# Kernel tuning notes

Hardware: AMD Instinct MI355X
Metric: run time of the kernel (lower is better)

Reference implementation:

```python
import jax, jax.numpy as jnp
import numpy as np

B, S, T, V, E, H, D, A = 16, 128, 128, 32000, 512, 512, 512, 512
ENC = 2 * H  # bidirectional encoder output dim
NEG = -1e9


def _w(key, shape, scale=0.05):
    return scale * jax.random.normal(key, shape, dtype=jnp.float32)


def setup_inputs() -> dict:
    key = jax.random.key(0)
    ks = jax.random.split(key, 26)
    src = jax.random.randint(ks[0], (B, S), 1, V)
    tgt = jax.random.randint(ks[1], (B, T), 1, V)
    src_lens = jnp.full((B,), S, dtype=jnp.int32)  # full-length sequences (pack == identity)
    return dict(
        src=src, src_lens=src_lens, tgt=tgt,
        enc_embed=_w(ks[2], (V, E)).at[0].set(0.0),   # padding_idx=0
        Wih_f=_w(ks[3], (4 * H, E)), Whh_f=_w(ks[4], (4 * H, H)),
        bih_f=_w(ks[5], (4 * H,)), bhh_f=_w(ks[6], (4 * H,)),
        Wih_b=_w(ks[7], (4 * H, E)), Whh_b=_w(ks[8], (4 * H, H)),
        bih_b=_w(ks[9], (4 * H,)), bhh_b=_w(ks[10], (4 * H,)),
        Wbh=_w(ks[11], (D, 2 * H)), bbh=_w(ks[12], (D,)),
        Wbc=_w(ks[13], (D, 2 * H)), bbc=_w(ks[14], (D,)),
        Wh_att=_w(ks[15], (A, ENC)), Ws_att=_w(ks[16], (A, D)), v_att=_w(ks[17], (A,)),
        dec_embed=_w(ks[18], (V, E)).at[0].set(0.0),  # padding_idx=0
        Wih_d=_w(ks[19], (4 * D, E + ENC)), Whh_d=_w(ks[20], (4 * D, D)),
        bih_d=_w(ks[21], (4 * D,)), bhh_d=_w(ks[22], (4 * D,)),
        Wfc=_w(ks[23], (V, D + ENC)), bfc=_w(ks[24], (V,)),
    )


def _lstm_cell(x, h, c, Wih, Whh, bih, bhh):
    # PyTorch gate order: i, f, g, o
    g = x @ Wih.T + h @ Whh.T + (bih + bhh)
    i, f, gg, o = jnp.split(g, 4, axis=-1)
    c = jax.nn.sigmoid(f) * c + jax.nn.sigmoid(i) * jnp.tanh(gg)
    h = jax.nn.sigmoid(o) * jnp.tanh(c)
    return h, c


def _run_lstm(xs, Wih, Whh, bih, bhh, hdim):
    # xs: [S, B, E] -> (hs [S, B, hdim], h_last, c_last)
    b = xs.shape[1]
    h0 = jnp.zeros((b, hdim), xs.dtype)

    def step(carry, x):
        h, c = carry
        h, c = _lstm_cell(x, h, c, Wih, Whh, bih, bhh)
        return (h, c), h

    (hT, cT), hs = jax.lax.scan(step, (h0, h0), xs)
    return hs, hT, cT


def reference(src, src_lens, tgt, enc_embed, Wih_f, Whh_f, bih_f, bhh_f,
              Wih_b, Whh_b, bih_b, bhh_b, Wbh, bbh, Wbc, bbc,
              Wh_att, Ws_att, v_att, dec_embed, Wih_d, Whh_d, bih_d, bhh_d,
              Wfc, bfc):
    # ---- BiLSTM encoder (src_lens == S, so packing is the identity) ----
    emb = enc_embed[src]                      # [B, S, E]
    xs = jnp.swapaxes(emb, 0, 1)              # [S, B, E]
    hs_f, hf, _ = _run_lstm(xs, Wih_f, Whh_f, bih_f, bhh_f, H)
    hs_b, hb, _ = _run_lstm(xs[::-1], Wih_b, Whh_b, bih_b, bhh_b, H)
    hs_b = hs_b[::-1]
    enc_out = jnp.swapaxes(jnp.concatenate([hs_f, hs_b], axis=-1), 0, 1)  # [B, S, 2H]

    # ---- bridge (num_layers = 1) ----
    h_cat = jnp.concatenate([hf, hb], axis=-1)  # [B, 2H]
    h0 = jnp.tanh(h_cat @ Wbh.T + bbh)          # [B, D]
    c_cat = jnp.concatenate([hf, hb], axis=-1)
    c0 = jnp.tanh(c_cat @ Wbc.T + bbc)

    mask = jnp.arange(S)[None, :] < src_lens[:, None]  # [B, S]
    enc_proj = jnp.einsum('bse,ae->bsa', enc_out, Wh_att)  # W_h(enc_out), hoisted

    # ---- decoder loop, teacher_forcing = 1.0 ----
    def dec_step(carry, inp_t):
        h, c = carry
        # Bahdanau attention on top-layer hidden state
        score = jnp.einsum('bsa,a->bs', jnp.tanh(enc_proj + (h @ Ws_att.T)[:, None, :]), v_att)
        score = jnp.where(mask, score, NEG)
        attn = jax.nn.softmax(score, axis=-1)
        ctx = jnp.einsum('bs,bse->be', attn, enc_out)       # [B, 2H]
        x = jnp.concatenate([dec_embed[inp_t], ctx], axis=-1)  # [B, E+2H]
        h, c = _lstm_cell(x, h, c, Wih_d, Whh_d, bih_d, bhh_d)
        logits = jnp.concatenate([h, ctx], axis=-1) @ Wfc.T + bfc  # [B, V]
        return (h, c), logits

    inps = tgt[:, :-1].T  # [T-1, B]
    _, logits = jax.lax.scan(dec_step, (h0, c0), inps)
    return jnp.swapaxes(logits, 0, 1)  # [B, T-1, V]
```

## Files before the change

### kernel.cpp

```cpp
#include <hip/hip_runtime.h>

typedef __bf16 bf16x8 __attribute__((ext_vector_type(8)));
typedef float f32x4 __attribute__((ext_vector_type(4)));
typedef unsigned short us;
typedef unsigned long long ull;

#define DEV static __device__ __forceinline__

DEV float bf2f(us u){ union { unsigned u; float f; } x; x.u = ((unsigned)u) << 16; return x.f; }
DEV us f2bf(float f){
  union { float f; unsigned u; } x; x.f = f;
  unsigned r = x.u + 0x7fffu + ((x.u >> 16) & 1u);
  return (us)(r >> 16);
}
DEV unsigned pack2(us lo, us hi){ return (unsigned)lo | ((unsigned)hi << 16); }
DEV float sigm(float x){ return 1.0f / (1.0f + expf(-x)); }
DEV float tanh_fast(float x){ float e = __expf(2.0f * x); return 1.0f - 2.0f / (e + 1.0f); }
DEV void unpk2(unsigned u, float& a, float& b){ a = bf2f((us)u); b = bf2f((us)(u >> 16)); }

DEV unsigned ld4v(const unsigned* p){ return __hip_atomic_load(p, __ATOMIC_RELAXED, __HIP_MEMORY_SCOPE_AGENT); }
DEV ull ld8v(const void* p){ return __hip_atomic_load((const ull*)p, __ATOMIC_RELAXED, __HIP_MEMORY_SCOPE_AGENT); }
DEV void st4v(unsigned* p, unsigned v){ __hip_atomic_store(p, v, __ATOMIC_RELAXED, __HIP_MEMORY_SCOPE_AGENT); }

DEV void gridbar3(unsigned* arr, unsigned ep){
  __syncthreads();
  if (threadIdx.x == 0)
    __hip_atomic_store(arr + (size_t)blockIdx.x * 16, ep, __ATOMIC_RELEASE, __HIP_MEMORY_SCOPE_AGENT);
  if (threadIdx.x < 128){
    while (__hip_atomic_load(arr + (size_t)threadIdx.x * 16, __ATOMIC_RELAXED, __HIP_MEMORY_SCOPE_AGENT) < ep)
      __builtin_amdgcn_s_sleep(4);
  }
  __syncthreads();
}

DEV void groupbar(unsigned* gbase, int slot, unsigned ep){
  __syncthreads();
  if (threadIdx.x == 0)
    __hip_atomic_store(gbase + slot * 16, ep, __ATOMIC_RELEASE, __HIP_MEMORY_SCOPE_AGENT);
  if (threadIdx.x < 8){
    while (__hip_atomic_load(gbase + threadIdx.x * 16, __ATOMIC_RELAXED, __HIP_MEMORY_SCOPE_AGENT) < ep)
      __builtin_amdgcn_s_sleep(2);
  }
  __syncthreads();
}

__global__ void k_f2bf(const float4* __restrict__ in, uint2* __restrict__ out, long n4){
  long stride = (long)gridDim.x * blockDim.x;
  for (long i = (long)blockIdx.x * blockDim.x + threadIdx.x; i < n4; i += stride){
    float4 v = in[i];
    uint2 o; o.x = pack2(f2bf(v.x), f2bf(v.y)); o.y = pack2(f2bf(v.z), f2bf(v.w));
    out[i] = o;
  }
}

__global__ void k_bias3(const float* a0, const float* b0, float* o0,
                        const float* a1, const float* b1, float* o1,
                        const float* a2, const float* b2, float* o2){
  int i = blockIdx.x * 256 + threadIdx.x;
  o0[i] = a0[i] + b0[i];
  o1[i] = a1[i] + b1[i];
  o2[i] = a2[i] + b2[i];
}

__global__ void k_embed(const int* __restrict__ tok, const float* __restrict__ table,
                        us* __restrict__ out){
  int r = blockIdx.x;
  int b = r & 15, pos = r >> 4;
  int idx = tok[b * 128 + pos];
  float4 v = ((const float4*)(table + (size_t)idx * 512))[threadIdx.x];
  uint2 o; o.x = pack2(f2bf(v.x), f2bf(v.y)); o.y = pack2(f2bf(v.z), f2bf(v.w));
  ((uint2*)(out + (size_t)r * 512))[threadIdx.x] = o;
}

template<int MODE>
__global__ __launch_bounds__(256)
void gemm_bt(const us* __restrict__ A, int lda,
             const us* __restrict__ B, int ldb,
             const float* __restrict__ bias,
             void* __restrict__ Cv, int ldc, int K, int mvalid)
{
  __shared__ __align__(16) us As[128 * 64];
  __shared__ __align__(16) us Bs[128 * 64];
  const int tid  = threadIdx.x;
  const int lane = tid & 63, wid = tid >> 6;
  const int wm = (wid >> 1) * 64, wn = (wid & 1) * 64;
  const us* Ab = A + (size_t)blockIdx.y * 128 * lda;
  const us* Bb = B + (size_t)blockIdx.x * 128 * ldb;

  f32x4 acc[4][4] = {};
  bf16x8 ga[4], gb[4];

  #pragma unroll
  for (int r = 0; r < 4; r++){
    int c = tid + r * 256;
    ga[r] = *(const bf16x8*)(Ab + (size_t)(c >> 3) * lda + (c & 7) * 8);
    gb[r] = *(const bf16x8*)(Bb + (size_t)(c >> 3) * ldb + (c & 7) * 8);
  }
  const int nt = K >> 6;
  for (int t = 0; t < nt; t++){
    #pragma unroll
    for (int r = 0; r < 4; r++){
      int c = tid + r * 256;
      int slot = ((c >> 3) * 8 + ((c & 7) ^ ((c >> 3) & 7))) * 8;
      *(bf16x8*)(As + slot) = ga[r];
      *(bf16x8*)(Bs + slot) = gb[r];
    }
    __syncthreads();
    if (t + 1 < nt){
      int k0 = (t + 1) * 64;
      #pragma unroll
      for (int r = 0; r < 4; r++){
        int c = tid + r * 256;
        ga[r] = *(const bf16x8*)(Ab + (size_t)(c >> 3) * lda + k0 + (c & 7) * 8);
        gb[r] = *(const bf16x8*)(Bb + (size_t)(c >> 3) * ldb + k0 + (c & 7) * 8);
      }
    }
    #pragma unroll
    for (int kk = 0; kk < 2; kk++){
      bf16x8 av[4], bv[4];
      #pragma unroll
      for (int i = 0; i < 4; i++){
        int ra = wm + i * 16 + (lane & 15);
        int ua = (kk * 4 + (lane >> 4)) ^ (ra & 7);
        av[i] = *(const bf16x8*)(As + (ra * 8 + ua) * 8);
        int rb = wn + i * 16 + (lane & 15);
        int ub = (kk * 4 + (lane >> 4)) ^ (rb & 7);
        bv[i] = *(const bf16x8*)(Bs + (rb * 8 + ub) * 8);
      }
      #pragma unroll
      for (int i = 0; i < 4; i++)
        #pragma unroll
        for (int j = 0; j < 4; j++)
          acc[i][j] = __builtin_amdgcn_mfma_f32_16x16x32_bf16(av[i], bv[j], acc[i][j], 0, 0, 0);
    }
    if (t + 1 < nt) __syncthreads();
  }

  const int cb = lane & 15, rb4 = (lane >> 4) * 4;
  #pragma unroll
  for (int i = 0; i < 4; i++){
    #pragma unroll
    for (int j = 0; j < 4; j++){
      #pragma unroll
      for (int r = 0; r < 4; r++){
        int row = blockIdx.y * 128 + wm + i * 16 + rb4 + r;
        int col = blockIdx.x * 128 + wn + j * 16 + cb;
        float v = acc[i][j][r];
        if (bias) v += bias[col];
        if (MODE == 0) ((float*)Cv)[(size_t)row * ldc + col] = v;
        else           ((us*)Cv)[(size_t)row * ldc + col] = f2bf(v);
      }
    }
  }
}

__global__ __launch_bounds__(256)
void enc_persist4(const float* __restrict__ gin_f, const float* __restrict__ gin_b,
                  const us* __restrict__ whhf_bf, const us* __restrict__ whhb_bf,
                  us* __restrict__ enc_out_bf,
                  unsigned* __restrict__ arr)
{
  __shared__ __align__(16) us Wt[2][1024][8];
  __shared__ __align__(16) us Hrow[2][16][520];
  __shared__ __align__(16) f32x4 P[2][4][64];
  __shared__ float gl[2][16][17];
  __shared__ float hvout[2][16][4];

  const int bx = blockIdx.x, tid = threadIdx.x;
  const int lane = tid & 63, wv = tid >> 6;

  for (int d = 0; d < 2; d++){
    const us* srcw = d ? whhb_bf : whhf_bf;
    for (int u = tid; u < 1024; u += 256){
      int ks = u >> 6, ch = (u >> 4) & 3, v = u & 15;
      int n = (v & 3) * 512 + bx * 4 + (v >> 2);
      *(bf16x8*)Wt[d][u] = *(const bf16x8*)(srcw + (size_t)n * 512 + ks * 32 + ch * 8);
    }
  }

  float creg = 0.0f;
  const int cd = (tid >> 6) & 1, cb = tid & 15, cj = (tid >> 4) & 3;

  for (int t = 0; t < 128; t++){
    if (t == 0){
      #pragma unroll
      for (int r = 0; r < 8; r++){
        int u = tid + r * 256;
        int d = u >> 10, b = (u >> 6) & 15, s16 = u & 63;
        *(ull*)&Hrow[d][b][s16 * 8]     = 0ull;
        *(ull*)&Hrow[d][b][s16 * 8 + 4] = 0ull;
      }
    } else {
      #pragma unroll
      for (int r = 0; r < 8; r++){
        int u = tid + r * 256;
        int d = u >> 10, b = (u >> 6) & 15, s16 = u & 63;
        int sp = d ? (128 - t) : (t - 1);
        const us* s = enc_out_bf + ((size_t)b * 128 + sp) * 1024 + d * 512 + s16 * 8;
        ull lo = ld8v(s), hi = ld8v(s + 4);
        *(ull*)&Hrow[d][b][s16 * 8]     = lo;
        *(ull*)&Hrow[d][b][s16 * 8 + 4] = hi;
      }
    }
    __syncthreads();
    #pragma unroll
    for (int d = 0; d < 2; d++){
      f32x4 acc = {};
      #pragma unroll
      for (int m = 0; m < 4; m++){
        int ks = wv * 4 + m;
        int ch = lane >> 4, b = lane & 15;
        acc = __builtin_amdgcn_mfma_f32_16x16x32_bf16(*(const bf16x8*)&Hrow[d][b][ks * 32 + ch * 8],
                                                      *(const bf16x8*)Wt[d][(ks * 4 + ch) * 16 + b],
                                                      acc, 0, 0, 0);
      }
      P[d][wv][lane] = acc;
    }
    __syncthreads();
    if (wv < 2){
      int d = wv;
      f32x4 sum = (P[d][0][lane] + P[d][1][lane]) + (P[d][2][lane] + P[d][3][lane]);
      int v = lane & 15;
      int n = (v & 3) * 512 + bx * 4 + (v >> 2);
      int s_in = d ? (127 - t) : t;
      const float* gg = (d ? gin_b : gin_f) + (size_t)s_in * 16 * 2048 + n;
      #pragma unroll
      for (int r = 0; r < 4; r++){
        int b = (lane >> 4) * 4 + r;
        gl[d][v][b] = sum[r] + gg[(size_t)b * 2048];
      }
    }
    __syncthreads();
    if (tid < 128){
      float ig = sigm (gl[cd][cj * 4 + 0][cb]);
      float fg = sigm (gl[cd][cj * 4 + 1][cb]);
      float g2 = tanhf(gl[cd][cj * 4 + 2][cb]);
      float og = sigm (gl[cd][cj * 4 + 3][cb]);
      float cn = fg * creg + ig * g2;
      float hv = og * tanhf(cn);
      creg = cn;
      hvout[cd][cb][cj] = hv;
    }
    __syncthreads();
    if (tid < 64){
      int d = tid >> 5, rem = tid & 31, b = rem & 15, jp = rem >> 4;
      int s_in = d ? (127 - t) : t;
      st4v((unsigned*)(enc_out_bf + ((size_t)b * 128 + s_in) * 1024 + d * 512 + bx * 4 + jp * 2),
           pack2(f2bf(hvout[d][b][jp * 2]), f2bf(hvout[d][b][jp * 2 + 1])));
    }
    if (t != 127) gridbar3(arr, t + 1);
  }
}

__global__ __launch_bounds__(512)
void k_h0c0(const us* __restrict__ enc_out_bf, const float* __restrict__ Wbh, const float* __restrict__ bbh,
            const float* __restrict__ Wbc, const float* __restrict__ bbc,
            us* __restrict__ h0_bf, float* __restrict__ c_dec)
{
  __shared__ float hc[1024];
  int b = blockIdx.x >> 1, which = blockIdx.x & 1;
  int tid = threadIdx.x;
  hc[tid]       = bf2f(enc_out_bf[((size_t)b * 128 + 127) * 1024 + tid]);
  hc[512 + tid] = bf2f(enc_out_bf[((size_t)b * 128 + 0)   * 1024 + 512 + tid]);
  __syncthreads();
  const float* W = which ? Wbc : Wbh;
  float acc = (which ? bbc : bbh)[tid];
  const float* wr = W + (size_t)tid * 1024;
  for (int k = 0; k < 1024; k += 4){
    float4 w = *(const float4*)(wr + k);
    acc += w.x * hc[k] + w.y * hc[k + 1] + w.z * hc[k + 2] + w.w * hc[k + 3];
  }
  float v = tanhf(acc);
  if (which) c_dec[b * 512 + tid] = v;
  else       h0_bf[b * 512 + tid] = f2bf(v);
}

#define SMEM_BYTES 148992

__global__ __launch_bounds__(256)
void dec_fused(const us* __restrict__ h0_bf, const float* __restrict__ c_dec0,
               const float* __restrict__ Ws_att, const float* __restrict__ v_att,
               const us* __restrict__ enc_proj_bf, const us* __restrict__ enc_out_bf,
               const int* __restrict__ src_lens, const float* __restrict__ gin_d,
               const us* __restrict__ whhd_bf, const us* __restrict__ wihd_bf,
               float* __restrict__ hs_g, float* __restrict__ esc_g,
               us* __restrict__ hctx,
               const us* __restrict__ wfc, const float* __restrict__ bfc,
               float* __restrict__ out,
               unsigned* __restrict__ arr, unsigned* __restrict__ arrG,
               unsigned* __restrict__ tdone)
{
  __shared__ __align__(16) char smem[SMEM_BYTES];
  const int tid = threadIdx.x;

  if (blockIdx.x >= 128){
    us* As = (us*)smem;
    us* Bs = (us*)(smem + 16384);
    const int lane = tid & 63, wid = tid >> 6;
    const int wm = (wid >> 1) * 64, wn = (wid & 1) * 64;
    for (int tile = blockIdx.x - 128; tile < 4000; tile += 128){
      int rt = tile / 250, ct = tile - rt * 250;
      unsigned need = (rt == 15) ? 127u : (unsigned)(8 * rt + 8);
      if (tid == 0){
        while (ld4v(tdone) < need) __builtin_amdgcn_s_sleep(8);
      }
      __syncthreads();
      const us* Ab = hctx + (size_t)rt * 128 * 1536;
      const us* Bb = wfc  + (size_t)ct * 128 * 1536;
      f32x4 acc[4][4] = {};
      bf16x8 ga[4], gb[4];
      #pragma unroll
      for (int r = 0; r < 4; r++){
        int cc = tid + r * 256;
        int row = cc >> 3, piece = cc & 7;
        bool val = (rt * 128 + row) < 2032;
        union { ull q[2]; bf16x8 v; } u;
        const us* p = Ab + (size_t)row * 1536 + piece * 8;
        u.q[0] = val ? ld8v(p) : 0ull;
        u.q[1] = val ? ld8v(p + 4) : 0ull;
        ga[r] = u.v;
        gb[r] = *(const bf16x8*)(Bb + (size_t)row * 1536 + piece * 8);
      }
      for (int tk = 0; tk < 24; tk++){
        #pragma unroll
        for (int r = 0; r < 4; r++){
          int cc = tid + r * 256;
          int slot = ((cc >> 3) * 8 + ((cc & 7) ^ ((cc >> 3) & 7))) * 8;
          *(bf16x8*)(As + slot) = ga[r];
          *(bf16x8*)(Bs + slot) = gb[r];
        }
        __syncthreads();
        if (tk + 1 < 24){
          int k0 = (tk + 1) * 64;
          #pragma unroll
          for (int r = 0; r < 4; r++){
            int cc = tid + r * 256;
            int row = cc >> 3, piece = cc & 7;
            bool val = (rt * 128 + row) < 2032;
            union { ull q[2]; bf16x8 v; } u;
            const us* p = Ab + (size_t)row * 1536 + k0 + piece * 8;
            u.q[0] = val ? ld8v(p) : 0ull;
            u.q[1] = val ? ld8v(p + 4) : 0ull;
            ga[r] = u.v;
            gb[r] = *(const bf16x8*)(Bb + (size_t)row * 1536 + k0 + piece * 8);
          }
        }
        #pragma unroll
        for (int kk = 0; kk < 2; kk++){
          bf16x8 av[4], bv[4];
          #pragma unroll
          for (int i = 0; i < 4; i++){
            int ra = wm + i * 16 + (lane & 15);
            int ua = (kk * 4 + (lane >> 4)) ^ (ra & 7);
            av[i] = *(const bf16x8*)(As + (ra * 8 + ua) * 8);
            int rb = wn + i * 16 + (lane & 15);
            int ub = (kk * 4 + (lane >> 4)) ^ (rb & 7);
            bv[i] = *(const bf16x8*)(Bs + (rb * 8 + ub) * 8);
          }
          #pragma unroll
          for (int i = 0; i < 4; i++)
            #pragma unroll
            for (int j = 0; j < 4; j++)
              acc[i][j] = __builtin_amdgcn_mfma_f32_16x16x32_bf16(av[i], bv[j], acc[i][j], 0, 0, 0);
        }
        if (tk + 1 < 24) __syncthreads();
      }
      const int cbl = lane & 15, rb4 = (lane >> 4) * 4;
      #pragma unroll
      for (int i = 0; i < 4; i++){
        #pragma unroll
        for (int j = 0; j < 4; j++){
          #pragma unroll
          for (int r = 0; r < 4; r++){
            int row = rt * 128 + wm + i * 16 + rb4 + r;
            int col = ct * 128 + wn + j * 16 + cbl;
            if (row < 2032){
              float v = acc[i][j][r] + bfc[col];
              int tt = row >> 4, b = row & 15;
              out[((size_t)b * 127 + tt) * 32000 + col] = v;
            }
          }
        }
      }
    }
    return;
  }

  us (*Wh)[8]      = (us(*)[8])(smem);
  us (*Wc)[8]      = (us(*)[8])(smem + 16384);
  us (*Ws_r)[512]  = (us(*)[512])(smem + 49152);
  us (*ep_r)[512]  = (us(*)[512])(smem + 53248);
  us (*eo_r)[128]  = (us(*)[128])(smem + 69632);
  us (*Xrow)[1032] = (us(*)[1032])(smem + 102400);
  f32x4 (*P)[64]   = (f32x4(*)[64])(smem + 135424);
  float (*g1l)[17] = (float(*)[17])(smem + 139520);
  float (*gl)[17]  = (float(*)[17])(smem + 140608);
  float* vl        = (float*)(smem + 141696);
  float (*hsp)[64] = (float(*)[64])(smem + 143744);
  float* hs_b      = (float*)(smem + 144768);
  float* att       = (float*)(smem + 146816);
  float (*cred)[128] = (float(*)[128])(smem + 147328);
  float* sred      = (float*)(smem + 148352);
  float (*hvs)[4]  = (float(*)[4])(smem + 148384);

  const int bx = blockIdx.x;
  const int lane = tid & 63, wv = tid >> 6;
  const int bB = bx & 15, sQ = bx >> 4;
  unsigned* gbase = arrG + bB * 128;

  for (int u = tid; u < 1024; u += 256){
    int ks = u >> 6, ch = (u >> 4) & 3, v = u & 15;
    int n = (v & 3) * 512 + bx * 4 + (v >> 2);
    *(bf16x8*)Wh[u] = *(const bf16x8*)(whhd_bf + (size_t)n * 512 + ks * 32 + ch * 8);
  }
  for (int u = tid; u < 2048; u += 256){
    int ks = u >> 6, ch = (u >> 4) & 3, v = u & 15;
    int n = (v & 3) * 512 + bx * 4 + (v >> 2);
    *(bf16x8*)Wc[u] = *(const bf16x8*)(wihd_bf + (size_t)n * 1536 + 512 + ks * 32 + ch * 8);
  }
  for (int u = tid; u < 2048; u += 256){
    int a = u >> 9, k = u & 511;
    Ws_r[a][k] = f2bf(Ws_att[(size_t)(bx * 4 + a) * 512 + k]);
  }
  for (int u = tid; u < 1024; u += 256){
    int si = u >> 6, a8 = (u & 63) * 8;
    *(bf16x8*)&ep_r[si][a8] =
      *(const bf16x8*)(enc_proj_bf + ((size_t)bB * 128 + sQ * 16 + si) * 512 + a8);
  }
  for (int u = tid; u < 2048; u += 256){
    int s = u >> 4, k8 = (u & 15) * 8;
    *(bf16x8*)&eo_r[s][k8] =
      *(const bf16x8*)(enc_out_bf + ((size_t)bB * 128 + s) * 1024 + sQ * 128 + k8);
  }
  for (int u = tid; u < 512; u += 256) vl[u] = v_att[u];
  const int slen = src_lens[bB];

  float creg = 0.0f;
  if (tid < 64) creg = c_dec0[(tid & 15) * 512 + bx * 4 + (tid >> 4)];

  for (int t = 0; t < 127; t++){
    const us* hsrc = t ? (hctx + (size_t)(t - 1) * 16 * 1536) : h0_bf;
    const int hstride = t ? 1536 : 512;

    #pragma unroll
    for (int r = 0; r < 4; r++){
      int u = tid + r * 256;
      int b = u >> 6, s16 = u & 63;
      const us* s = hsrc + (size_t)b * hstride + s16 * 8;
      ull lo = ld8v(s), hi = ld8v(s + 4);
      *(ull*)&Xrow[b][s16 * 8]     = lo;
      *(ull*)&Xrow[b][s16 * 8 + 4] = hi;
    }
    __syncthreads();
    {
      f32x4 acc = {};
      #pragma unroll
      for (int m = 0; m < 4; m++){
        int ks = wv * 4 + m;
        int ch = lane >> 4, b = lane & 15;
        acc = __builtin_amdgcn_mfma_f32_16x16x32_bf16(*(const bf16x8*)&Xrow[b][ks * 32 + ch * 8],
                                                      *(const bf16x8*)Wh[(ks * 4 + ch) * 16 + b],
                                                      acc, 0, 0, 0);
      }
      P[wv][lane] = acc;
    }
    {
      int pr = tid & 63, bq = pr & 15, ai = pr >> 4, kq = wv;
      const us* wr = Ws_r[ai] + kq * 128;
      const us* xr = Xrow[bq] + kq * 128;
      float s = 0.f;
      #pragma unroll
      for (int k = 0; k < 128; k += 8){
        bf16x8 xv = *(const bf16x8*)(xr + k);
        bf16x8 wv8 = *(const bf16x8*)(wr + k);
        #pragma unroll
        for (int e = 0; e < 8; e++) s += (float)xv[e] * (float)wv8[e];
      }
      hsp[kq][pr] = s;
    }
    __syncthreads();
    if (wv == 0){
      f32x4 sum = (P[0][lane] + P[1][lane]) + (P[2][lane] + P[3][lane]);
      int v = lane & 15;
      int n = (v & 3) * 512 + bx * 4 + (v >> 2);
      #pragma unroll
      for (int r = 0; r < 4; r++){
        int b = (lane >> 4) * 4 + r;
        g1l[v][b] = sum[r] + gin_d[((size_t)t * 16 + b) * 2048 + n];
      }
    }
    if (tid < 64){
      float v = hsp[0][tid] + hsp[1][tid] + hsp[2][tid] + hsp[3][tid];
      st4v((unsigned*)&hs_g[(tid & 15) * 512 + bx * 4 + (tid >> 4)], __float_as_uint(v));
    }

    gridbar3(arr, 3 * t + 1);

    {
      ull v = ld8v(&hs_g[bB * 512 + tid * 2]);
      *(ull*)&hs_b[tid * 2] = v;
    }
    __syncthreads();
    {
      int si = tid >> 4, part = tid & 15;
      const us* er = ep_r[si] + part * 32;
      const float* hb = hs_b + part * 32;
      const float* vp = vl + part * 32;
      float sv = 0.f;
      #pragma unroll
      for (int a = 0; a < 32; a += 8){
        uint4 u4 = *(const uint4*)(er + a);
        float e0,e1,e2,e3,e4,e5,e6,e7;
        unpk2(u4.x,e0,e1); unpk2(u4.y,e2,e3); unpk2(u4.z,e4,e5); unpk2(u4.w,e6,e7);
        sv += vp[a+0]*tanh_fast(e0+hb[a+0]) + vp[a+1]*tanh_fast(e1+hb[a+1])
            + vp[a+2]*tanh_fast(e2+hb[a+2]) + vp[a+3]*tanh_fast(e3+hb[a+3])
            + vp[a+4]*tanh_fast(e4+hb[a+4]) + vp[a+5]*tanh_fast(e5+hb[a+5])
            + vp[a+6]*tanh_fast(e6+hb[a+6]) + vp[a+7]*tanh_fast(e7+hb[a+7]);
      }
      sv += __shfl_xor(sv, 1);
      sv += __shfl_xor(sv, 2);
      sv += __shfl_xor(sv, 4);
      sv += __shfl_xor(sv, 8);
      if (part == 0){
        int s = sQ * 16 + si;
        float e = (s < slen) ? __expf(sv) : 0.f;
        st4v((unsigned*)&esc_g[bB * 128 + s], __float_as_uint(e));
      }
    }

    groupbar(gbase, sQ, t + 1);

    {
      float e = 0.f;
      if (tid < 128) e = __uint_as_float(ld4v((unsigned*)&esc_g[bB * 128 + tid]));
      if (tid < 128) att[tid] = e;
      float ss = e;
      #pragma unroll
      for (int o = 32; o; o >>= 1) ss += __shfl_xor(ss, o);
      if (lane == 0) sred[wv] = ss;
    }
    __syncthreads();
    {
      int kk = tid & 127, half = tid >> 7;
      const float* ab = att + half * 64;
      const us* er = &eo_r[half * 64][kk];
      float s = 0.f;
      #pragma unroll 8
      for (int s2 = 0; s2 < 64; s2++)
        s += ab[s2] * bf2f(er[(size_t)s2 * 128]);
      cred[half][kk] = s;
    }
    __syncthreads();
    if (tid < 64){
      float inv = 1.0f / (sred[0] + sred[1] + sred[2] + sred[3]);
      int kk2 = tid * 2;
      float c0 = (cred[0][kk2]     + cred[1][kk2])     * inv;
      float c1 = (cred[0][kk2 + 1] + cred[1][kk2 + 1]) * inv;
      st4v((unsigned*)(hctx + ((size_t)t * 16 + bB) * 1536 + 512 + sQ * 128 + kk2),
           pack2(f2bf(c0), f2bf(c1)));
    }

    gridbar3(arr, 3 * t + 2);

    #pragma unroll
    for (int r = 0; r < 8; r++){
      int u = tid + r * 256;
      int b = u >> 7, s16 = u & 127;
      const us* s = hctx + ((size_t)t * 16 + b) * 1536 + 512 + s16 * 8;
      ull lo = ld8v(s), hi = ld8v(s + 4);
      *(ull*)&Xrow[b][s16 * 8]     = lo;
      *(ull*)&Xrow[b][s16 * 8 + 4] = hi;
    }
    __syncthreads();
    {
      f32x4 acc = {};
      #pragma unroll
      for (int m = 0; m < 8; m++){
        int ks = wv * 8 + m;
        int ch = lane >> 4, b = lane & 15;
        acc = __builtin_amdgcn_mfma_f32_16x16x32_bf16(*(const bf16x8*)&Xrow[b][ks * 32 + ch * 8],
                                                      *(const bf16x8*)Wc[(ks * 4 + ch) * 16 + b],
                                                      acc, 0, 0, 0);
      }
      P[wv][lane] = acc;
    }
    __syncthreads();
    if (wv == 0){
      f32x4 sum = (P[0][lane] + P[1][lane]) + (P[2][lane] + P[3][lane]);
      int v = lane & 15;
      #pragma unroll
      for (int r = 0; r < 4; r++){
        int b = (lane >> 4) * 4 + r;
        gl[v][b] = sum[r] + g1l[v][b];
      }
    }
    __syncthreads();
    if (tid < 64){
      int b2 = tid & 15, joff = tid >> 4;
      float ig = sigm (gl[joff * 4 + 0][b2]);
      float fg = sigm (gl[joff * 4 + 1][b2]);
      float g2 = tanhf(gl[joff * 4 + 2][b2]);
      float og = sigm (gl[joff * 4 + 3][b2]);
      float cn = fg * creg + ig * g2;
      float hv = og * tanhf(cn);
      creg = cn;
      hvs[b2][joff] = hv;
    }
    __syncthreads();
    if (tid < 32){
      int b = tid & 15, jp = tid >> 4;
      st4v((unsigned*)(hctx + ((size_t)t * 16 + b) * 1536 + bx * 4 + jp * 2),
           pack2(f2bf(hvs[b][jp * 2]), f2bf(hvs[b][jp * 2 + 1])));
    }
    gridbar3(arr, 3 * t + 3);
    if (bx == 0 && tid == 0)
      __hip_atomic_store(tdone, (unsigned)(t + 1), __ATOMIC_RELEASE, __HIP_MEMORY_SCOPE_AGENT);
  }
}

extern "C" void kernel_launch(void* const* d_in, const int* in_sizes, int n_in,
                              void* d_out, int out_size, void* d_ws, size_t ws_size,
                              hipStream_t stream)
{
  const int*   src       = (const int*)d_in[0];
  const int*   src_lens  = (const int*)d_in[1];
  const int*   tgt       = (const int*)d_in[2];
  const float* enc_embed = (const float*)d_in[3];
  const float* Wih_f = (const float*)d_in[4];
  const float* Whh_f = (const float*)d_in[5];
  const float* bih_f = (const float*)d_in[6];
  const float* bhh_f = (const float*)d_in[7];
  const float* Wih_b = (const float*)d_in[8];
  const float* Whh_b = (const float*)d_in[9];
  const float* bih_b = (const float*)d_in[10];
  const float* bhh_b = (const float*)d_in[11];
  const float* Wbh = (const float*)d_in[12];
  const float* bbh = (const float*)d_in[13];
  const float* Wbc = (const float*)d_in[14];
  const float* bbc = (const float*)d_in[15];
  const float* Wh_att = (const float*)d_in[16];
  const float* Ws_att = (const float*)d_in[17];
  const float* v_att  = (const float*)d_in[18];
  const float* dec_embed = (const float*)d_in[19];
  const float* Wih_d = (const float*)d_in[20];
  const float* Whh_d = (const float*)d_in[21];
  const float* bih_d = (const float*)d_in[22];
  const float* bhh_d = (const float*)d_in[23];
  const float* Wfc = (const float*)d_in[24];
  const float* bfc = (const float*)d_in[25];
  float* out = (float*)d_out;

  char* base = (char*)d_ws;
  size_t off = 0;
  auto take = [&](size_t bytes) -> char* {
    char* p = base + off;
    off += (bytes + 255) & ~(size_t)255;
    return p;
  };
  us* wfc_bf    = (us*)take((size_t)32000 * 1536 * 2);
  us* emb_e     = (us*)take((size_t)2048 * 512 * 2);
  us* emb_d     = (us*)take((size_t)2048 * 512 * 2);
  us* wihf_bf   = (us*)take((size_t)2048 * 512 * 2);
  us* wihb_bf   = (us*)take((size_t)2048 * 512 * 2);
  us* wihd_bf   = (us*)take((size_t)2048 * 1536 * 2);
  us* whhf_bf   = (us*)take((size_t)2048 * 512 * 2);
  us* whhb_bf   = (us*)take((size_t)2048 * 512 * 2);
  us* whhd_bf   = (us*)take((size_t)2048 * 512 * 2);
  us* whatt_bf  = (us*)take((size_t)512 * 1024 * 2);
  float* gin_f    = (float*)take((size_t)2048 * 2048 * 4);
  float* gin_b    = (float*)take((size_t)2048 * 2048 * 4);
  float* gin_d    = (float*)take((size_t)2048 * 2048 * 4);
  us* enc_out_bf  = (us*)take((size_t)2048 * 1024 * 2);
  us* enc_proj_bf = (us*)take((size_t)2048 * 512 * 2);
  us* hctx        = (us*)take((size_t)2048 * 1536 * 2);
  us* h0_bf       = (us*)take((size_t)16 * 512 * 2);
  float* c_dec    = (float*)take((size_t)16 * 512 * 4);
  float* hs_g     = (float*)take((size_t)16 * 512 * 4);
  float* esc_g    = (float*)take((size_t)16 * 128 * 4);
  float* bias_f = (float*)take(2048 * 4);
  float* bias_b = (float*)take(2048 * 4);
  float* bias_d = (float*)take(2048 * 4);
  unsigned* arrE  = (unsigned*)take(128 * 16 * 4);
  unsigned* arrD  = (unsigned*)take(128 * 16 * 4);
  unsigned* arrG  = (unsigned*)take(16 * 8 * 16 * 4);
  unsigned* tdone = (unsigned*)take(256);

  hipMemsetAsync(emb_d, 0, (size_t)2048 * 512 * 2, stream);
  hipMemsetAsync(hctx, 0, (size_t)2048 * 1536 * 2, stream);
  hipMemsetAsync(arrE, 0, (128 * 16 + 128 * 16 + 16 * 8 * 16) * 4 + 256, stream);

  k_f2bf<<<4096, 256, 0, stream>>>((const float4*)Wfc,   (uint2*)wfc_bf,   (long)32000 * 1536 / 4);
  k_f2bf<<<512,  256, 0, stream>>>((const float4*)Wih_f, (uint2*)wihf_bf,  (long)2048 * 512 / 4);
  k_f2bf<<<512,  256, 0, stream>>>((const float4*)Wih_b, (uint2*)wihb_bf,  (long)2048 * 512 / 4);
  k_f2bf<<<1024, 256, 0, stream>>>((const float4*)Wih_d, (uint2*)wihd_bf,  (long)2048 * 1536 / 4);
  k_f2bf<<<512,  256, 0, stream>>>((const float4*)Whh_f, (uint2*)whhf_bf,  (long)2048 * 512 / 4);
  k_f2bf<<<512,  256, 0, stream>>>((const float4*)Whh_b, (uint2*)whhb_bf,  (long)2048 * 512 / 4);
  k_f2bf<<<512,  256, 0, stream>>>((const float4*)Whh_d, (uint2*)whhd_bf,  (long)2048 * 512 / 4);
  k_f2bf<<<512,  256, 0, stream>>>((const float4*)Wh_att,(uint2*)whatt_bf, (long)512 * 1024 / 4);
  k_bias3<<<8, 256, 0, stream>>>(bih_f, bhh_f, bias_f, bih_b, bhh_b, bias_b, bih_d, bhh_d, bias_d);

  k_embed<<<2048, 128, 0, stream>>>(src, enc_embed, emb_e);
  k_embed<<<2032, 128, 0, stream>>>(tgt, dec_embed, emb_d);

  gemm_bt<0><<<dim3(16, 16), 256, 0, stream>>>(emb_e, 512, wihf_bf, 512,  bias_f, gin_f, 2048, 512, 4096);
  gemm_bt<0><<<dim3(16, 16), 256, 0, stream>>>(emb_e, 512, wihb_bf, 512,  bias_b, gin_b, 2048, 512, 4096);
  gemm_bt<0><<<dim3(16, 16), 256, 0, stream>>>(emb_d, 512, wihd_bf, 1536, bias_d, gin_d, 2048, 512, 4096);

  enc_persist4<<<128, 256, 0, stream>>>(gin_f, gin_b, whhf_bf, whhb_bf, enc_out_bf, arrE);

  k_h0c0<<<32, 512, 0, stream>>>(enc_out_bf, Wbh, bbh, Wbc, bbc, h0_bf, c_dec);

  gemm_bt<2><<<dim3(4, 16), 256, 0, stream>>>(enc_out_bf, 1024, whatt_bf, 1024, nullptr, enc_proj_bf, 512, 1024, 4096);

  dec_fused<<<256, 256, 0, stream>>>(h0_bf, c_dec, Ws_att, v_att, enc_proj_bf, enc_out_bf, src_lens,
                                     gin_d, whhd_bf, wihd_bf, hs_g, esc_g, hctx,
                                     wfc_bf, bfc, out, arrD, arrG, tdone);
}
```

Baseline: 3.859 ms.

## Replace per-step grid barrier with group barrier and enlarge logits GEMM tiles

Each decoder block now computes the 64-column slice of h@Ws_att for its own batch row, so the attention hidden projection only needs a per-batch group barrier instead of a full grid barrier. This cuts grid barriers per step from three to two. The logits GEMM blocks switch to 256x128 tiles, which halves the tile count and improves operand reuse. To fit the larger Ws slice in shared memory, enc_proj and enc_out rows are now read from global memory each step instead of being cached in LDS, which adds global traffic.

```diff
diff --git a/kernel.cpp b/kernel.cpp
--- a/kernel.cpp
+++ b/kernel.cpp
@@ -275,92 +275,108 @@
   else       h0_bf[b * 512 + tid] = f2bf(v);
 }
 
-#define SMEM_BYTES 148992
+#define SMEM_BYTES 161952
 
 __global__ __launch_bounds__(256)
-void dec_fused(const us* __restrict__ h0_bf, const float* __restrict__ c_dec0,
-               const float* __restrict__ Ws_att, const float* __restrict__ v_att,
-               const us* __restrict__ enc_proj_bf, const us* __restrict__ enc_out_bf,
-               const int* __restrict__ src_lens, const float* __restrict__ gin_d,
-               const us* __restrict__ whhd_bf, const us* __restrict__ wihd_bf,
-               float* __restrict__ hs_g, float* __restrict__ esc_g,
-               us* __restrict__ hctx,
-               const us* __restrict__ wfc, const float* __restrict__ bfc,
-               float* __restrict__ out,
-               unsigned* __restrict__ arr, unsigned* __restrict__ arrG,
-               unsigned* __restrict__ tdone)
+void dec_fused2(const us* __restrict__ h0_bf, const float* __restrict__ c_dec0,
+                const float* __restrict__ Ws_att, const float* __restrict__ v_att,
+                const us* __restrict__ enc_proj_bf, const us* __restrict__ enc_out_bf,
+                const int* __restrict__ src_lens, const float* __restrict__ gin_d,
+                const us* __restrict__ whhd_bf, const us* __restrict__ wihd_bf,
+                float* __restrict__ hs_g, float* __restrict__ esc_g,
+                us* __restrict__ hctx,
+                const us* __restrict__ wfc, const float* __restrict__ bfc,
+                float* __restrict__ out,
+                unsigned* __restrict__ arr, unsigned* __restrict__ arrG,
+                unsigned* __restrict__ tdone)
 {
   __shared__ __align__(16) char smem[SMEM_BYTES];
   const int tid = threadIdx.x;
 
   if (blockIdx.x >= 128){
     us* As = (us*)smem;
-    us* Bs = (us*)(smem + 16384);
+    us* Bs = (us*)(smem + 32768);
     const int lane = tid & 63, wid = tid >> 6;
-    const int wm = (wid >> 1) * 64, wn = (wid & 1) * 64;
-    for (int tile = blockIdx.x - 128; tile < 4000; tile += 128){
+    const int wm = wid * 64;
+    for (int tile = blockIdx.x - 128; tile < 2000; tile += 128){
       int rt = tile / 250, ct = tile - rt * 250;
-      unsigned need = (rt == 15) ? 127u : (unsigned)(8 * rt + 8);
+      unsigned need = (rt == 7) ? 127u : (unsigned)(16 * rt + 16);
       if (tid == 0){
         while (ld4v(tdone) < need) __builtin_amdgcn_s_sleep(8);
       }
       __syncthreads();
-      const us* Ab = hctx + (size_t)rt * 128 * 1536;
+      const us* Ab = hctx + (size_t)rt * 256 * 1536;
       const us* Bb = wfc  + (size_t)ct * 128 * 1536;
-      f32x4 acc[4][4] = {};
-      bf16x8 ga[4], gb[4];
-      #pragma unroll
-      for (int r = 0; r < 4; r++){
+      f32x4 acc[4][8] = {};
+      bf16x8 ga[8], gb[4];
+      #pragma unroll
+      for (int r = 0; r < 8; r++){
         int cc = tid + r * 256;
         int row = cc >> 3, piece = cc & 7;
-        bool val = (rt * 128 + row) < 2032;
+        bool val = (rt * 256 + row) < 2032;
         union { ull q[2]; bf16x8 v; } u;
         const us* p = Ab + (size_t)row * 1536 + piece * 8;
         u.q[0] = val ? ld8v(p) : 0ull;
         u.q[1] = val ? ld8v(p + 4) : 0ull;
         ga[r] = u.v;
-        gb[r] = *(const bf16x8*)(Bb + (size_t)row * 1536 + piece * 8);
+      }
+      #pragma unroll
+      for (int r = 0; r < 4; r++){
+        int cc = tid + r * 256;
+        gb[r] = *(const bf16x8*)(Bb + (size_t)(cc >> 3) * 1536 + (cc & 7) * 8);
       }
       for (int tk = 0; tk < 24; tk++){
+        #pragma unroll
+        for (int r = 0; r < 8; r++){
+          int cc = tid + r * 256;
+          int slot = ((cc >> 3) * 8 + ((cc & 7) ^ ((cc >> 3) & 7))) * 8;
+          *(bf16x8*)(As + slot) = ga[r];
+        }
         #pragma unroll
         for (int r = 0; r < 4; r++){
           int cc = tid + r * 256;
           int slot = ((cc >> 3) * 8 + ((cc & 7) ^ ((cc >> 3) & 7))) * 8;
-          *(bf16x8*)(As + slot) = ga[r];
           *(bf16x8*)(Bs + slot) = gb[r];
         }
         __syncthreads();
         if (tk + 1 < 24){
           int k0 = (tk + 1) * 64;
           #pragma unroll
-          for (int r = 0; r < 4; r++){
+          for (int r = 0; r < 8; r++){
             int cc = tid + r * 256;
             int row = cc >> 3, piece = cc & 7;
-            bool val = (rt * 128 + row) < 2032;
+            bool val = (rt * 256 + row) < 2032;
             union { ull q[2]; bf16x8 v; } u;
             const us* p = Ab + (size_t)row * 1536 + k0 + piece * 8;
             u.q[0] = val ? ld8v(p) : 0ull;
             u.q[1] = val ? ld8v(p + 4) : 0ull;
             ga[r] = u.v;
-            gb[r] = *(const bf16x8*)(Bb + (size_t)row * 1536 + k0 + piece * 8);
+          }
+          #pragma unroll
+          for (int r = 0; r < 4; r++){
+            int cc = tid + r * 256;
+            gb[r] = *(const bf16x8*)(Bb + (size_t)(cc >> 3) * 1536 + k0 + (cc & 7) * 8);
           }
         }
         #pragma unroll
         for (int kk = 0; kk < 2; kk++){
-          bf16x8 av[4], bv[4];
+          bf16x8 av[4], bv[8];
           #pragma unroll
           for (int i = 0; i < 4; i++){
             int ra = wm + i * 16 + (lane & 15);
             int ua = (kk * 4 + (lane >> 4)) ^ (ra & 7);
             av[i] = *(const bf16x8*)(As + (ra * 8 + ua) * 8);
-            int rb = wn + i * 16 + (lane & 15);
+          }
+          #pragma unroll
+          for (int j = 0; j < 8; j++){
+            int rb = j * 16 + (lane & 15);
             int ub = (kk * 4 + (lane >> 4)) ^ (rb & 7);
-            bv[i] = *(const bf16x8*)(Bs + (rb * 8 + ub) * 8);
+            bv[j] = *(const bf16x8*)(Bs + (rb * 8 + ub) * 8);
           }
           #pragma unroll
           for (int i = 0; i < 4; i++)
             #pragma unroll
-            for (int j = 0; j < 4; j++)
+            for (int j = 0; j < 8; j++)
               acc[i][j] = __builtin_amdgcn_mfma_f32_16x16x32_bf16(av[i], bv[j], acc[i][j], 0, 0, 0);
         }
         if (tk + 1 < 24) __syncthreads();
@@ -369,11 +385,11 @@
       #pragma unroll
       for (int i = 0; i < 4; i++){
         #pragma unroll
-        for (int j = 0; j < 4; j++){
+        for (int j = 0; j < 8; j++){
           #pragma unroll
           for (int r = 0; r < 4; r++){
-            int row = rt * 128 + wm + i * 16 + rb4 + r;
-            int col = ct * 128 + wn + j * 16 + cbl;
+            int row = rt * 256 + wm + i * 16 + rb4 + r;
+            int col = ct * 128 + j * 16 + cbl;
             if (row < 2032){
               float v = acc[i][j][r] + bfc[col];
               int tt = row >> 4, b = row & 15;
@@ -388,20 +404,18 @@
 
   us (*Wh)[8]      = (us(*)[8])(smem);
   us (*Wc)[8]      = (us(*)[8])(smem + 16384);
-  us (*Ws_r)[512]  = (us(*)[512])(smem + 49152);
-  us (*ep_r)[512]  = (us(*)[512])(smem + 53248);
-  us (*eo_r)[128]  = (us(*)[128])(smem + 69632);
-  us (*Xrow)[1032] = (us(*)[1032])(smem + 102400);
-  f32x4 (*P)[64]   = (f32x4(*)[64])(smem + 135424);
-  float (*g1l)[17] = (float(*)[17])(smem + 139520);
-  float (*gl)[17]  = (float(*)[17])(smem + 140608);
-  float* vl        = (float*)(smem + 141696);
-  float (*hsp)[64] = (float(*)[64])(smem + 143744);
-  float* hs_b      = (float*)(smem + 144768);
-  float* att       = (float*)(smem + 146816);
-  float (*cred)[128] = (float(*)[128])(smem + 147328);
-  float* sred      = (float*)(smem + 148352);
-  float (*hvs)[4]  = (float(*)[4])(smem + 148384);
+  us (*Ws64)[520]  = (us(*)[520])(smem + 49152);
+  us (*Xrow)[1032] = (us(*)[1032])(smem + 115712);
+  f32x4 (*P)[64]   = (f32x4(*)[64])(smem + 148736);
+  float (*g1l)[17] = (float(*)[17])(smem + 152832);
+  float (*gl)[17]  = (float(*)[17])(smem + 153920);
+  float* vl        = (float*)(smem + 155008);
+  float (*hsp)[64] = (float(*)[64])(smem + 157056);
+  float* hs_b      = (float*)(smem + 158080);
+  float* att       = (float*)(smem + 160128);
+  float (*cred)[128] = (float(*)[128])(smem + 160640);
+  float* sred      = (float*)(smem + 161664);
+  float (*hvs)[4]  = (float(*)[4])(smem + 161696);
 
   const int bx = blockIdx.x;
   const int lane = tid & 63, wv = tid >> 6;
@@ -418,19 +432,9 @@
     int n = (v & 3) * 512 + bx * 4 + (v >> 2);
     *(bf16x8*)Wc[u] = *(const bf16x8*)(wihd_bf + (size_t)n * 1536 + 512 + ks * 32 + ch * 8);
   }
-  for (int u = tid; u < 2048; u += 256){
+  for (int u = tid; u < 32768; u += 256){
     int a = u >> 9, k = u & 511;
-    Ws_r[a][k] = f2bf(Ws_att[(size_t)(bx * 4 + a) * 512 + k]);
-  }
-  for (int u = tid; u < 1024; u += 256){
-    int si = u >> 6, a8 = (u & 63) * 8;
-    *(bf16x8*)&ep_r[si][a8] =
-      *(const bf16x8*)(enc_proj_bf + ((size_t)bB * 128 + sQ * 16 + si) * 512 + a8);
-  }
-  for (int u = tid; u < 2048; u += 256){
-    int s = u >> 4, k8 = (u & 15) * 8;
-    *(bf16x8*)&eo_r[s][k8] =
-      *(const bf16x8*)(enc_out_bf + ((size_t)bB * 128 + s) * 1024 + sQ * 128 + k8);
+    Ws64[a][k] = f2bf(Ws_att[(size_t)(sQ * 64 + a) * 512 + k]);
   }
   for (int u = tid; u < 512; u += 256) vl[u] = v_att[u];
   const int slen = src_lens[bB];
@@ -465,9 +469,8 @@
       P[wv][lane] = acc;
     }
     {
-      int pr = tid & 63, bq = pr & 15, ai = pr >> 4, kq = wv;
-      const us* wr = Ws_r[ai] + kq * 128;
-      const us* xr = Xrow[bq] + kq * 128;
+      const us* wr = Ws64[lane] + wv * 128;
+      const us* xr = Xrow[bB] + wv * 128;
       float s = 0.f;
       #pragma unroll
       for (int k = 0; k < 128; k += 8){
@@ -476,7 +479,7 @@
         #pragma unroll
         for (int e = 0; e < 8; e++) s += (float)xv[e] * (float)wv8[e];
       }
-      hsp[kq][pr] = s;
+      hsp[wv][lane] = s;
     }
     __syncthreads();
     if (wv == 0){
@@ -491,10 +494,10 @@
     }
     if (tid < 64){
       float v = hsp[0][tid] + hsp[1][tid] + hsp[2][tid] + hsp[3][tid];
-      st4v((unsigned*)&hs_g[(tid & 15) * 512 + bx * 4 + (tid >> 4)], __float_as_uint(v));
-    }
-
-    gridbar3(arr, 3 * t + 1);
+      st4v((unsigned*)&hs_g[bB * 512 + sQ * 64 + tid], __float_as_uint(v));
+    }
+
+    groupbar(gbase, sQ, 2 * t + 1);
 
     {
       ull v = ld8v(&hs_g[bB * 512 + tid * 2]);
@@ -503,7 +506,7 @@
     __syncthreads();
     {
       int si = tid >> 4, part = tid & 15;
-      const us* er = ep_r[si] + part * 32;
+      const us* er = enc_proj_bf + ((size_t)bB * 128 + sQ * 16 + si) * 512 + part * 32;
       const float* hb = hs_b + part * 32;
       const float* vp = vl + part * 32;
       float sv = 0.f;
@@ -528,7 +531,7 @@
       }
     }
 
-    groupbar(gbase, sQ, t + 1);
+    groupbar(gbase, sQ, 2 * t + 2);
 
     {
       float e = 0.f;
@@ -543,11 +546,11 @@
     {
       int kk = tid & 127, half = tid >> 7;
       const float* ab = att + half * 64;
-      const us* er = &eo_r[half * 64][kk];
+      const us* er = enc_out_bf + ((size_t)(bB * 128 + half * 64)) * 1024 + sQ * 128 + kk;
       float s = 0.f;
       #pragma unroll 8
       for (int s2 = 0; s2 < 64; s2++)
-        s += ab[s2] * bf2f(er[(size_t)s2 * 128]);
+        s += ab[s2] * bf2f(er[(size_t)s2 * 1024]);
       cred[half][kk] = s;
     }
     __syncthreads();
@@ -560,7 +563,7 @@
            pack2(f2bf(c0), f2bf(c1)));
     }
 
-    gridbar3(arr, 3 * t + 2);
+    gridbar3(arr, 2 * t + 1);
 
     #pragma unroll
     for (int r = 0; r < 8; r++){
@@ -612,7 +615,7 @@
       st4v((unsigned*)(hctx + ((size_t)t * 16 + b) * 1536 + bx * 4 + jp * 2),
            pack2(f2bf(hvs[b][jp * 2]), f2bf(hvs[b][jp * 2 + 1])));
     }
-    gridbar3(arr, 3 * t + 3);
+    gridbar3(arr, 2 * t + 2);
     if (bx == 0 && tid == 0)
       __hip_atomic_store(tdone, (unsigned)(t + 1), __ATOMIC_RELEASE, __HIP_MEMORY_SCOPE_AGENT);
   }
@@ -712,7 +715,7 @@
 
   gemm_bt<2><<<dim3(4, 16), 256, 0, stream>>>(enc_out_bf, 1024, whatt_bf, 1024, nullptr, enc_proj_bf, 512, 1024, 4096);
 
-  dec_fused<<<256, 256, 0, stream>>>(h0_bf, c_dec, Ws_att, v_att, enc_proj_bf, enc_out_bf, src_lens,
-                                     gin_d, whhd_bf, wihd_bf, hs_g, esc_g, hctx,
-                                     wfc_bf, bfc, out, arrD, arrG, tdone);
-}
+  dec_fused2<<<256, 256, 0, stream>>>(h0_bf, c_dec, Ws_att, v_att, enc_proj_bf, enc_out_bf, src_lens,
+                                      gin_d, whhd_bf, wihd_bf, hs_g, esc_g, hctx,
+                                      wfc_bf, bfc, out, arrD, arrG, tdone);
+}
```

Result: no change. 3.866 ms (+0.2%).
